# Performance work log

Measured on AMD Instinct MI355X. Metric: run time of the kernel, lower is better.

## Reference

```python
import jax, jax.numpy as jnp
import numpy as np

HIDDEN = 1024
HEADS = 16
HEAD_DIM = HIDDEN // HEADS
B, S = 2, 2048


def setup_inputs() -> dict:
    key = jax.random.key(0)
    k1, k2, k3 = jax.random.split(key, 3)
    x = jax.random.normal(k1, (B, S, HIDDEN), dtype=jnp.float32)
    qkv_w = jax.random.normal(k2, (3 * HIDDEN, HIDDEN), dtype=jnp.float32) * (HIDDEN ** -0.5)
    out_w = jax.random.normal(k3, (HIDDEN, HIDDEN), dtype=jnp.float32) * (HIDDEN ** -0.5)
    return {"x": x, "qkv_w": qkv_w, "out_w": out_w}


def reference(x, qkv_w, out_w):
    b, s, d = x.shape
    scale = HEAD_DIM ** -0.5
    # qkv projection (Linear without bias: x @ W^T)
    qkv = x @ qkv_w.T                                   # [b, s, 3d]
    qkv = qkv.reshape(b, s, 3, HEADS, HEAD_DIM)
    qkv = jnp.transpose(qkv, (2, 0, 3, 1, 4))           # [3, b, h, s, hd]
    q, k, v = qkv[0] * scale, qkv[1], qkv[2]
    # causal attention (blocked torch loop == full causal softmax attention)
    scores = jnp.einsum('bhqd,bhkd->bhqk', q, k)        # [b, h, s, s]
    causal = jnp.tril(jnp.ones((s, s), dtype=bool))
    scores = jnp.where(causal[None, None], scores, -jnp.inf)
    weights = jax.nn.softmax(scores, axis=-1)
    attn = jnp.einsum('bhqk,bhkd->bhqd', weights, v)    # [b, h, s, hd]
    attn = jnp.transpose(attn, (0, 2, 1, 3)).reshape(b, s, d)
    return attn @ out_w.T
```

## Files before the change

kernel.cpp:

```cpp
#include <hip/hip_runtime.h>
#include <hip/hip_bf16.h>
#include <math.h>

#define HIDDEN 1024
#define HEADS 16
#define HDIM 64
#define BATCH 2
#define SEQ 2048
#define BHN (BATCH*HEADS)
#define MTOT (BATCH*SEQ)

typedef __attribute__((ext_vector_type(8))) short short8;
typedef __attribute__((ext_vector_type(4))) short short4v;
typedef __attribute__((ext_vector_type(4))) float floatx4;

#define GL2LDS(gsrc, ldst) __builtin_amdgcn_global_load_lds( \
    (const __attribute__((address_space(1))) void*)(gsrc), \
    (__attribute__((address_space(3))) void*)(ldst), 16, 0, 0)

__device__ __forceinline__ short f2bf(float f) {
  union { float f; unsigned u; } v; v.f = f;
  unsigned u = v.u;
  unsigned r = (u + 0x7fffu + ((u >> 16) & 1u)) >> 16;
  return (short)r;
}

__global__ __launch_bounds__(256) void cvt3_f32_bf16(
    const float* __restrict__ a, const float* __restrict__ b, const float* __restrict__ c,
    short* __restrict__ oa, short* __restrict__ ob, short* __restrict__ oc) {
  int i = blockIdx.x * 256 + threadIdx.x;
  const float* src; short* dst; int j;
  if (i < 1048576)      { src = a; dst = oa; j = i; }
  else if (i < 1835008) { src = b; dst = ob; j = i - 1048576; }
  else                  { src = c; dst = oc; j = i - 1835008; }
  float4 f = reinterpret_cast<const float4*>(src)[j];
  short4 o;
  o.x = f2bf(f.x); o.y = f2bf(f.y); o.z = f2bf(f.z); o.w = f2bf(f.w);
  reinterpret_cast<short4*>(dst)[j] = o;
}

template<int EPI, int BN>
__global__ __launch_bounds__(256) void gemm_bt(
    const short* __restrict__ A, const short* __restrict__ B,
    int M, int N, int K,
    float* __restrict__ outF,
    short* __restrict__ outQ, short* __restrict__ outK, short* __restrict__ outV)
{
  constexpr int WN = BN / 2;
  constexpr int NI = BN / 32;
  __shared__ __align__(16) short As[128*64];
  __shared__ __align__(16) short Bs[BN*64];
  const int tid = threadIdx.x;
  const int wv = tid >> 6;
  const int lane = tid & 63;
  const int l15 = lane & 15;
  const int quad = lane >> 4;
  const int swl = l15 & 7;
  const int wm = wv >> 1, wn = wv & 1;
  const int row0 = blockIdx.y * 128, col0 = blockIdx.x * BN;

  floatx4 acc[4][NI];
#pragma unroll
  for (int i = 0; i < 4; i++)
#pragma unroll
    for (int j = 0; j < NI; j++) acc[i][j] = (floatx4){0.f, 0.f, 0.f, 0.f};

  for (int k0 = 0; k0 < K; k0 += 64) {
#pragma unroll
    for (int rd = 0; rd < 4; ++rd) {
      int chunk = rd * 256 + tid;
      int r = chunk >> 3, c = ((chunk & 7) ^ (r & 7)) << 3;
      GL2LDS(A + (long)(row0 + r) * K + k0 + c, As + (rd * 256 + wv * 64) * 8);
    }
#pragma unroll
    for (int rd = 0; rd < BN / 32; ++rd) {
      int chunk = rd * 256 + tid;
      int r = chunk >> 3, c = ((chunk & 7) ^ (r & 7)) << 3;
      GL2LDS(B + (long)(col0 + r) * K + k0 + c, Bs + (rd * 256 + wv * 64) * 8);
    }
    __syncthreads();

    short8 af[4][2], bfr[NI][2];
#pragma unroll
    for (int mi = 0; mi < 4; mi++) {
      const short* ap = As + (wm * 64 + mi * 16 + l15) * 64;
#pragma unroll
      for (int kk = 0; kk < 2; kk++)
        af[mi][kk] = *(const short8*)(ap + (((kk * 4 + quad) ^ swl) << 3));
    }
#pragma unroll
    for (int ni = 0; ni < NI; ni++) {
      const short* bp = Bs + (wn * WN + ni * 16 + l15) * 64;
#pragma unroll
      for (int kk = 0; kk < 2; kk++)
        bfr[ni][kk] = *(const short8*)(bp + (((kk * 4 + quad) ^ swl) << 3));
    }
#pragma unroll
    for (int mi = 0; mi < 4; mi++)
#pragma unroll
      for (int ni = 0; ni < NI; ni++)
#pragma unroll
        for (int kk = 0; kk < 2; kk++)
          acc[mi][ni] = __builtin_amdgcn_mfma_f32_16x16x32_bf16(af[mi][kk], bfr[ni][kk], acc[mi][ni], 0, 0, 0);
    __syncthreads();
  }

  if (EPI == 2) {
#pragma unroll
    for (int mi = 0; mi < 4; mi++) {
      int rr = row0 + wm * 64 + mi * 16 + quad * 4;
#pragma unroll
      for (int ni = 0; ni < NI; ni++) {
        int cc = col0 + wn * WN + ni * 16 + l15;
#pragma unroll
        for (int r = 0; r < 4; r++)
          outF[(long)(rr + r) * N + cc] = acc[mi][ni][r];
      }
    }
  } else {
#pragma unroll
    for (int mi = 0; mi < 4; mi++) {
      int rowg = row0 + wm * 64 + mi * 16 + quad * 4;
#pragma unroll
      for (int ni = 0; ni < NI; ni++) {
        int j = col0 + wn * WN + ni * 16 + l15;
        int t = j >> 10;
        int rem = j & 1023;
        int h = rem >> 6, d = rem & 63;
#pragma unroll
        for (int r = 0; r < 4; r++) {
          int i = rowg + r;
          int b = i >> 11, s = i & 2047;
          int bh = b * HEADS + h;
          float v = acc[mi][ni][r];
          if (t == 0)      outQ[(bh * SEQ + s) * HDIM + d] = f2bf(v * 0.18033688011112042f);
          else if (t == 1) outK[(bh * SEQ + s) * HDIM + d] = f2bf(v);
          else             outV[(bh * HDIM + d) * SEQ + s] = f2bf(v);
        }
      }
    }
  }
}

__device__ __forceinline__ void stage_kv(const short* __restrict__ kg,
                                         const short* __restrict__ vT,
                                         int bh, int kt, short* KsB, short* VsB,
                                         int tid, int wv) {
#pragma unroll
  for (int i = 0; i < 4; ++i) {
    int slot = i * 128 + tid;
    int r = slot >> 3;
    int sc = ((slot & 7) ^ (r & 7)) << 3;
    GL2LDS(kg + (bh * SEQ + kt * 64 + r) * HDIM + sc, KsB + (i * 128 + wv * 64) * 8);
    GL2LDS(vT + (bh * HDIM + r) * SEQ + kt * 64 + sc, VsB + (i * 128 + wv * 64) * 8);
  }
}

__global__ __launch_bounds__(128, 2) void flash_attn(
    const short* __restrict__ qg, const short* __restrict__ kg,
    const short* __restrict__ vT, short* __restrict__ attn)
{
  __shared__ __align__(16) short Ks[2][64 * 64];
  __shared__ __align__(16) short Vs[2][64 * 64];

  const int tid = threadIdx.x;
  const int wv = tid >> 6, lane = tid & 63;
  const int l15 = lane & 15, quad = lane >> 4;
  const int bh = blockIdx.x;
  const int rt = 31 - (int)blockIdx.y;
  const int m0 = rt * 64 + wv * 32;
  const int swl = l15 & 7;

  short8 aq[2][2];
#pragma unroll
  for (int mi = 0; mi < 2; mi++) {
    const short* qp = qg + (long)(bh * SEQ + m0 + mi * 16 + l15) * HDIM + quad * 8;
    aq[mi][0] = *(const short8*)qp;
    aq[mi][1] = *(const short8*)(qp + 32);
  }

  const short ONE = (short)0x3F80;
  const short4v ones4 = {ONE, ONE, ONE, ONE};

  floatx4 o[2][4], lsum[2];
#pragma unroll
  for (int mi = 0; mi < 2; mi++) {
    lsum[mi] = (floatx4){0.f, 0.f, 0.f, 0.f};
#pragma unroll
    for (int nt = 0; nt < 4; nt++) o[mi][nt] = (floatx4){0.f, 0.f, 0.f, 0.f};
  }

  const int ntiles = rt + 1;
  stage_kv(kg, vT, bh, 0, Ks[0], Vs[0], tid, wv);

  for (int kt = 0; kt < ntiles; ++kt) {
    __syncthreads();
    const int buf = kt & 1;
    if (kt + 1 < ntiles)
      stage_kv(kg, vT, bh, kt + 1, Ks[buf ^ 1], Vs[buf ^ 1], tid, wv);

    const short* KsB = Ks[buf];
    const short* VsB = Vs[buf];

    floatx4 sc[2][4];
#pragma unroll
    for (int mi = 0; mi < 2; mi++)
#pragma unroll
      for (int nh = 0; nh < 4; nh++) sc[mi][nh] = (floatx4){0.f, 0.f, 0.f, 0.f};
#pragma unroll
    for (int nh = 0; nh < 4; nh++) {
      const short* kp = KsB + (nh * 16 + l15) * 64;
      short8 kf0 = *(const short8*)(kp + ((quad ^ swl) << 3));
      short8 kf1 = *(const short8*)(kp + (((4 + quad) ^ swl) << 3));
#pragma unroll
      for (int mi = 0; mi < 2; mi++) {
        sc[mi][nh] = __builtin_amdgcn_mfma_f32_16x16x32_bf16(kf0, aq[mi][0], sc[mi][nh], 0, 0, 0);
        sc[mi][nh] = __builtin_amdgcn_mfma_f32_16x16x32_bf16(kf1, aq[mi][1], sc[mi][nh], 0, 0, 0);
      }
    }

    short4v pa[2][4];
#pragma unroll
    for (int mi = 0; mi < 2; mi++) {
      const int qrow = m0 + mi * 16 + l15;
      const bool full = (kt * 64 + 63) <= (m0 + mi * 16);
#pragma unroll
      for (int nh = 0; nh < 4; nh++) {
        unsigned u[4];
#pragma unroll
        for (int r = 0; r < 4; r++) {
          float pe = __builtin_amdgcn_exp2f(sc[mi][nh][r]);
          if (!full) {
            const int kpos = kt * 64 + nh * 16 + quad * 4 + r;
            pe = (kpos <= qrow) ? pe : 0.f;
          }
          u[r] = __builtin_bit_cast(unsigned, pe) & 0xffff0000u;
        }
        uint2 w;
        w.x = (u[0] >> 16) | u[1];
        w.y = (u[2] >> 16) | u[3];
        pa[mi][nh] = __builtin_bit_cast(short4v, w);
      }
    }

#pragma unroll
    for (int kk = 0; kk < 4; kk++) {
      short4v bv[4];
#pragma unroll
      for (int nt = 0; nt < 4; nt++) {
        const int ch = (kk * 2 + (quad >> 1)) ^ swl;
        bv[nt] = *(const short4v*)(VsB + (nt * 16 + l15) * 64 + (ch << 3) + ((quad & 1) << 2));
      }
#pragma unroll
      for (int mi = 0; mi < 2; mi++) {
        lsum[mi] = __builtin_amdgcn_mfma_f32_16x16x16bf16_1k(pa[mi][kk], ones4, lsum[mi], 0, 0, 0);
#pragma unroll
        for (int nt = 0; nt < 4; nt++)
          o[mi][nt] = __builtin_amdgcn_mfma_f32_16x16x16bf16_1k(pa[mi][kk], bv[nt], o[mi][nt], 0, 0, 0);
      }
    }
  }

  const int b = bh >> 4, h = bh & 15;
#pragma unroll
  for (int mi = 0; mi < 2; mi++)
#pragma unroll
    for (int r = 0; r < 4; r++) {
      const float inv = 1.0f / lsum[mi][r];
      const int s = m0 + mi * 16 + quad * 4 + r;
#pragma unroll
      for (int nt = 0; nt < 4; nt++)
        attn[(long)(b * SEQ + s) * HIDDEN + h * HDIM + nt * 16 + l15] = f2bf(o[mi][nt][r] * inv);
    }
}

extern "C" void kernel_launch(void* const* d_in, const int* in_sizes, int n_in,
                              void* d_out, int out_size, void* d_ws, size_t ws_size,
                              hipStream_t stream) {
  const float* x     = (const float*)d_in[0];
  const float* qkv_w = (const float*)d_in[1];
  const float* out_w = (const float*)d_in[2];
  float* out = (float*)d_out;

  short* xb   = (short*)d_ws;
  short* wqb  = xb  + MTOT * HIDDEN;
  short* wob  = wqb + 3 * HIDDEN * HIDDEN;
  short* qB   = wob + HIDDEN * HIDDEN;
  short* kB   = qB  + BHN * SEQ * HDIM;
  short* vTB  = kB  + BHN * SEQ * HDIM;
  short* attn = vTB + BHN * SEQ * HDIM;

  cvt3_f32_bf16<<<dim3(8192), dim3(256), 0, stream>>>(x, qkv_w, out_w, xb, wqb, wob);

  gemm_bt<1, 128><<<dim3(3 * HIDDEN / 128, MTOT / 128), dim3(256), 0, stream>>>(
      xb, wqb, MTOT, 3 * HIDDEN, HIDDEN, nullptr, qB, kB, vTB);

  flash_attn<<<dim3(BHN, SEQ / 64), dim3(128), 0, stream>>>(qB, kB, vTB, attn);

  gemm_bt<2, 64><<<dim3(HIDDEN / 64, MTOT / 128), dim3(256), 0, stream>>>(
      attn, wob, MTOT, HIDDEN, HIDDEN, out, nullptr, nullptr, nullptr);
}
```

Measured before the change: 181.7 us.

## Split flash attention tile across four waves and reorder causal tile scheduling

The attention block grows from 2 to 4 wavefronts, each owning 16 query rows instead of 32, so per-wave register state halves and more waves share each staged K/V tile. Occupancy is raised via launch bounds (256,4). The block-to-row-tile mapping is permuted in groups of 8 with alternating direction, to balance the long and short causal tiles across concurrently running blocks. The trade-off is that each wave loses the reuse of K/V LDS fragments across two M sub-tiles, so LDS reads per MFMA roughly double.

```diff
diff --git a/kernel.cpp b/kernel.cpp
--- a/kernel.cpp
+++ b/kernel.cpp
@@ -147,16 +147,16 @@
                                          int bh, int kt, short* KsB, short* VsB,
                                          int tid, int wv) {
 #pragma unroll
-  for (int i = 0; i < 4; ++i) {
-    int slot = i * 128 + tid;
+  for (int i = 0; i < 2; ++i) {
+    int slot = i * 256 + tid;
     int r = slot >> 3;
-    int sc = ((slot & 7) ^ (r & 7)) << 3;
-    GL2LDS(kg + (bh * SEQ + kt * 64 + r) * HDIM + sc, KsB + (i * 128 + wv * 64) * 8);
-    GL2LDS(vT + (bh * HDIM + r) * SEQ + kt * 64 + sc, VsB + (i * 128 + wv * 64) * 8);
-  }
-}
-
-__global__ __launch_bounds__(128, 2) void flash_attn(
+    int c = ((slot & 7) ^ (r & 7)) << 3;
+    GL2LDS(kg + (bh * SEQ + kt * 64 + r) * HDIM + c, KsB + (i * 256 + wv * 64) * 8);
+    GL2LDS(vT + (bh * HDIM + r) * SEQ + kt * 64 + c, VsB + (i * 256 + wv * 64) * 8);
+  }
+}
+
+__global__ __launch_bounds__(256, 4) void flash_attn(
     const short* __restrict__ qg, const short* __restrict__ kg,
     const short* __restrict__ vT, short* __restrict__ attn)
 {
@@ -167,28 +167,26 @@
   const int wv = tid >> 6, lane = tid & 63;
   const int l15 = lane & 15, quad = lane >> 4;
   const int bh = blockIdx.x;
-  const int rt = 31 - (int)blockIdx.y;
-  const int m0 = rt * 64 + wv * 32;
+  const int yl = (int)blockIdx.y;
+  const int sgrp = yl >> 3, y0 = yl & 7;
+  const int yp = ((sgrp >> 1) << 4) + ((sgrp & 1) ? (15 - y0) : y0);
+  const int rt = 31 - yp;
+  const int m0 = rt * 64 + wv * 16;
   const int swl = l15 & 7;
 
-  short8 aq[2][2];
-#pragma unroll
-  for (int mi = 0; mi < 2; mi++) {
-    const short* qp = qg + (long)(bh * SEQ + m0 + mi * 16 + l15) * HDIM + quad * 8;
-    aq[mi][0] = *(const short8*)qp;
-    aq[mi][1] = *(const short8*)(qp + 32);
+  short8 aq[2];
+  {
+    const short* qp = qg + (long)(bh * SEQ + m0 + l15) * HDIM + quad * 8;
+    aq[0] = *(const short8*)qp;
+    aq[1] = *(const short8*)(qp + 32);
   }
 
   const short ONE = (short)0x3F80;
   const short4v ones4 = {ONE, ONE, ONE, ONE};
 
-  floatx4 o[2][4], lsum[2];
-#pragma unroll
-  for (int mi = 0; mi < 2; mi++) {
-    lsum[mi] = (floatx4){0.f, 0.f, 0.f, 0.f};
-#pragma unroll
-    for (int nt = 0; nt < 4; nt++) o[mi][nt] = (floatx4){0.f, 0.f, 0.f, 0.f};
-  }
+  floatx4 o[4], lsum = (floatx4){0.f, 0.f, 0.f, 0.f};
+#pragma unroll
+  for (int nt = 0; nt < 4; nt++) o[nt] = (floatx4){0.f, 0.f, 0.f, 0.f};
 
   const int ntiles = rt + 1;
   stage_kv(kg, vT, bh, 0, Ks[0], Vs[0], tid, wv);
@@ -202,45 +200,37 @@
     const short* KsB = Ks[buf];
     const short* VsB = Vs[buf];
 
-    floatx4 sc[2][4];
-#pragma unroll
-    for (int mi = 0; mi < 2; mi++)
-#pragma unroll
-      for (int nh = 0; nh < 4; nh++) sc[mi][nh] = (floatx4){0.f, 0.f, 0.f, 0.f};
+    floatx4 sc4[4];
+#pragma unroll
+    for (int nh = 0; nh < 4; nh++) sc4[nh] = (floatx4){0.f, 0.f, 0.f, 0.f};
 #pragma unroll
     for (int nh = 0; nh < 4; nh++) {
       const short* kp = KsB + (nh * 16 + l15) * 64;
       short8 kf0 = *(const short8*)(kp + ((quad ^ swl) << 3));
       short8 kf1 = *(const short8*)(kp + (((4 + quad) ^ swl) << 3));
-#pragma unroll
-      for (int mi = 0; mi < 2; mi++) {
-        sc[mi][nh] = __builtin_amdgcn_mfma_f32_16x16x32_bf16(kf0, aq[mi][0], sc[mi][nh], 0, 0, 0);
-        sc[mi][nh] = __builtin_amdgcn_mfma_f32_16x16x32_bf16(kf1, aq[mi][1], sc[mi][nh], 0, 0, 0);
-      }
-    }
-
-    short4v pa[2][4];
-#pragma unroll
-    for (int mi = 0; mi < 2; mi++) {
-      const int qrow = m0 + mi * 16 + l15;
-      const bool full = (kt * 64 + 63) <= (m0 + mi * 16);
-#pragma unroll
-      for (int nh = 0; nh < 4; nh++) {
-        unsigned u[4];
-#pragma unroll
-        for (int r = 0; r < 4; r++) {
-          float pe = __builtin_amdgcn_exp2f(sc[mi][nh][r]);
-          if (!full) {
-            const int kpos = kt * 64 + nh * 16 + quad * 4 + r;
-            pe = (kpos <= qrow) ? pe : 0.f;
-          }
-          u[r] = __builtin_bit_cast(unsigned, pe) & 0xffff0000u;
+      sc4[nh] = __builtin_amdgcn_mfma_f32_16x16x32_bf16(kf0, aq[0], sc4[nh], 0, 0, 0);
+      sc4[nh] = __builtin_amdgcn_mfma_f32_16x16x32_bf16(kf1, aq[1], sc4[nh], 0, 0, 0);
+    }
+
+    short4v pa[4];
+    const int qrow = m0 + l15;
+    const bool full = (kt * 64 + 63) <= m0;
+#pragma unroll
+    for (int nh = 0; nh < 4; nh++) {
+      unsigned u[4];
+#pragma unroll
+      for (int r = 0; r < 4; r++) {
+        float pe = __builtin_amdgcn_exp2f(sc4[nh][r]);
+        if (!full) {
+          const int kpos = kt * 64 + nh * 16 + quad * 4 + r;
+          pe = (kpos <= qrow) ? pe : 0.f;
         }
-        uint2 w;
-        w.x = (u[0] >> 16) | u[1];
-        w.y = (u[2] >> 16) | u[3];
-        pa[mi][nh] = __builtin_bit_cast(short4v, w);
-      }
+        u[r] = __builtin_bit_cast(unsigned, pe) & 0xffff0000u;
+      }
+      uint2 w;
+      w.x = (u[0] >> 16) | u[1];
+      w.y = (u[2] >> 16) | u[3];
+      pa[nh] = __builtin_bit_cast(short4v, w);
     }
 
 #pragma unroll
@@ -251,27 +241,22 @@
         const int ch = (kk * 2 + (quad >> 1)) ^ swl;
         bv[nt] = *(const short4v*)(VsB + (nt * 16 + l15) * 64 + (ch << 3) + ((quad & 1) << 2));
       }
-#pragma unroll
-      for (int mi = 0; mi < 2; mi++) {
-        lsum[mi] = __builtin_amdgcn_mfma_f32_16x16x16bf16_1k(pa[mi][kk], ones4, lsum[mi], 0, 0, 0);
-#pragma unroll
-        for (int nt = 0; nt < 4; nt++)
-          o[mi][nt] = __builtin_amdgcn_mfma_f32_16x16x16bf16_1k(pa[mi][kk], bv[nt], o[mi][nt], 0, 0, 0);
-      }
+      lsum = __builtin_amdgcn_mfma_f32_16x16x16bf16_1k(pa[kk], ones4, lsum, 0, 0, 0);
+#pragma unroll
+      for (int nt = 0; nt < 4; nt++)
+        o[nt] = __builtin_amdgcn_mfma_f32_16x16x16bf16_1k(pa[kk], bv[nt], o[nt], 0, 0, 0);
     }
   }
 
   const int b = bh >> 4, h = bh & 15;
 #pragma unroll
-  for (int mi = 0; mi < 2; mi++)
-#pragma unroll
-    for (int r = 0; r < 4; r++) {
-      const float inv = 1.0f / lsum[mi][r];
-      const int s = m0 + mi * 16 + quad * 4 + r;
-#pragma unroll
-      for (int nt = 0; nt < 4; nt++)
-        attn[(long)(b * SEQ + s) * HIDDEN + h * HDIM + nt * 16 + l15] = f2bf(o[mi][nt][r] * inv);
-    }
+  for (int r = 0; r < 4; r++) {
+    const float inv = 1.0f / lsum[r];
+    const int srow = m0 + quad * 4 + r;
+#pragma unroll
+    for (int nt = 0; nt < 4; nt++)
+      attn[(long)(b * SEQ + srow) * HIDDEN + h * HDIM + nt * 16 + l15] = f2bf(o[nt][r] * inv);
+  }
 }
 
 extern "C" void kernel_launch(void* const* d_in, const int* in_sizes, int n_in,
@@ -295,7 +280,7 @@
   gemm_bt<1, 128><<<dim3(3 * HIDDEN / 128, MTOT / 128), dim3(256), 0, stream>>>(
       xb, wqb, MTOT, 3 * HIDDEN, HIDDEN, nullptr, qB, kB, vTB);
 
-  flash_attn<<<dim3(BHN, SEQ / 64), dim3(128), 0, stream>>>(qB, kB, vTB, attn);
+  flash_attn<<<dim3(BHN, SEQ / 64), dim3(256), 0, stream>>>(qB, kB, vTB, attn);
 
   gemm_bt<2, 64><<<dim3(HIDDEN / 64, MTOT / 128), dim3(256), 0, stream>>>(
       attn, wob, MTOT, HIDDEN, HIDDEN, out, nullptr, nullptr, nullptr);
```

Result: faster. 176.3 us (-3.0%).
